# Kernel tuning notes

Measured on AMD Instinct MI355X. Metric: run time of the kernel, lower is better.

The kernel has to match this reference:

```python
import jax, jax.numpy as jnp
import numpy as np

B, S, F = 128, 32, 128
N_ACT = 19


def build_edge_index(S):
    """4-neighbor grid edges (directed both ways) + bidirectional meta-node edges."""
    idx = np.arange(S * S).reshape(S, S)
    src = np.concatenate([idx[:, :-1].ravel(), idx[:, 1:].ravel(), idx[:-1, :].ravel(), idx[1:, :].ravel()])
    dst = np.concatenate([idx[:, 1:].ravel(), idx[:, :-1].ravel(), idx[1:, :].ravel(), idx[:-1, :].ravel()])
    meta = S * S
    cells = np.arange(S * S)
    src = np.concatenate([src, cells, np.full(S * S, meta)])
    dst = np.concatenate([dst, np.full(S * S, meta), cells])
    return src.astype(np.int32), dst.astype(np.int32)


def setup_inputs() -> dict:
    key = jax.random.key(0)
    ks = jax.random.split(key, 16)
    g = lambda k, shape, fan: jax.random.normal(k, shape, jnp.float32) * (0.5 / np.sqrt(fan))
    return {
        "gmap": jax.random.normal(ks[0], (B, S, S, F), jnp.float32),
        "pos": jax.random.randint(ks[1], (B, 2), 0, S, jnp.int32),
        "action_mask": jax.random.randint(ks[2], (B, N_ACT), 0, 2, jnp.int32),
        "Ws": g(ks[3], (3, 128, 128), 128),
        "Wn": g(ks[4], (3, 128, 128), 128),
        "bs": jnp.zeros((3, 128), jnp.float32),
        "W_d1": g(ks[5], (640, 512), 640), "b_d1": jnp.zeros((512,), jnp.float32),
        "W_d2": g(ks[6], (512, 512), 512), "b_d2": jnp.zeros((512,), jnp.float32),
        "W_d3": g(ks[7], (512, 256), 512), "b_d3": jnp.zeros((256,), jnp.float32),
        "W_p1": g(ks[8], (256, 256), 256), "b_p1": jnp.zeros((256,), jnp.float32),
        "W_p2": g(ks[9], (256, 256), 256), "b_p2": jnp.zeros((256,), jnp.float32),
        "W_p3": g(ks[10], (256, 19), 256), "b_p3": jnp.zeros((19,), jnp.float32),
    }


def reference(gmap, pos, action_mask, Ws, Wn, bs,
              W_d1, b_d1, W_d2, b_d2, W_d3, b_d3,
              W_p1, b_p1, W_p2, b_p2, W_p3, b_p3):
    Bb, Ss = gmap.shape[0], gmap.shape[1]
    Ff = gmap.shape[3]
    src, dst = build_edge_index(Ss)  # constant edge structure (cache in original)
    # flatten map -> nodes, append zero meta node
    x = gmap.reshape(Bb, Ss * Ss, Ff)
    x = jnp.concatenate([x, jnp.zeros((Bb, 1, Ff), x.dtype)], axis=1)  # [B, N, F]
    # GNN tower: self + neighbor-sum message passing, ELU
    for l in range(Ws.shape[0]):
        agg = jnp.zeros_like(x).at[:, dst].add(x[:, src])  # scatter-add over edges
        x = jax.nn.elu(x @ Ws[l] + agg @ Wn[l] + bs[l])
    emb = x[:, :-1, :]  # drop meta node -> [B, S*S, D]
    D = emb.shape[-1]
    # pick_from_map: pad spatially by 1, gather 5 cells (N,W,S,E,center)
    m = emb.reshape(Bb, Ss, Ss, D)
    mpf = jnp.pad(m, ((0, 0), (1, 1), (1, 1), (0, 0))).reshape(Bb, (Ss + 2) * (Ss + 2), D)
    offsets = jnp.array([(-1, 0), (0, -1), (1, 0), (0, 1), (0, 0)], jnp.float32)
    o_pos = pos.astype(jnp.float32)[:, None, :] + offsets + 1.0  # [B, 5, 2]
    # NOTE: original uses stride map_size (S), not S+2, on the padded flat array
    j = (o_pos @ jnp.array([float(Ss), 1.0], jnp.float32)).astype(jnp.int32)  # [B, 5]
    picked = jnp.take_along_axis(mpf, j[:, :, None], axis=1)  # [B, 5, D]
    state = picked.reshape(Bb, 5 * D)
    # directions MLP
    h = jax.nn.elu(state @ W_d1 + b_d1)
    h = jax.nn.elu(h @ W_d2 + b_d2)
    feat = jax.nn.elu(h @ W_d3 + b_d3)
    # policy head + action mask
    p = jax.nn.elu(feat @ W_p1 + b_p1)
    p = jax.nn.elu(p @ W_p2 + b_p2)
    logits = p @ W_p3 + b_p3
    inf_mask = jnp.maximum(jnp.log(action_mask.astype(jnp.float32)),
                           jnp.finfo(jnp.float32).min)
    return logits + inf_mask
```

## Files before the change

### kernel.cpp

```cpp
#include <hip/hip_runtime.h>
#include <hip/hip_bf16.h>

#define BATCH 128
#define SGRID 32
#define NCELL 1024
#define NTOT  1025
#define FD    128
#define NACT  19
#define NEG_INF_F  (-3.4028234663852886e38f)
#define BF16_SAFE_F (3.3e38f)
#define XSTR 136

typedef unsigned short ushort_t;
typedef unsigned int   uint_t;
typedef short   short8   __attribute__((ext_vector_type(8)));
typedef float   floatx16 __attribute__((ext_vector_type(16)));

__device__ __forceinline__ float elu_fast(float v) {
    return v > 0.f ? v : (__expf(v) - 1.f);
}
__device__ __forceinline__ float bf2f(ushort_t h) {
    union { uint_t u; float f; } v; v.u = ((uint_t)h) << 16; return v.f;
}
__device__ __forceinline__ ushort_t f2bf(float f) {
    union { float f; uint_t u; } v; v.f = f;
    uint_t r = v.u + 0x7FFFu + ((v.u >> 16) & 1u);
    return (ushort_t)(r >> 16);
}
__device__ __forceinline__ uint_t pkbf(float a, float b) {
    union { __hip_bfloat162 h; uint_t u; } v;
    v.h = __float22bfloat162_rn(make_float2(a, b));
    return v.u;
}
__device__ __forceinline__ void unpack2(uint_t u, float& a, float& b) {
    union { uint_t x; float f; } lo, hi;
    lo.x = u << 16; hi.x = u & 0xFFFF0000u;
    a = lo.f; b = hi.f;
}
__device__ __forceinline__ void unpack8(uint4 v, float* f) {
    unpack2(v.x, f[0], f[1]); unpack2(v.y, f[2], f[3]);
    unpack2(v.z, f[4], f[5]); unpack2(v.w, f[6], f[7]);
}
__device__ __forceinline__ void unpack4(uint2 v, float* f) {
    unpack2(v.x, f[0], f[1]); unpack2(v.y, f[2], f[3]);
}

__global__ __launch_bounds__(256) void setup_kernel(
    const ushort_t* __restrict__ Ws,
    const ushort_t* __restrict__ Wn,
    ushort_t* __restrict__ wfrag,
    float* __restrict__ s0s1)
{
    const int g = blockIdx.x * 256 + threadIdx.x;
    if (g < 4096) {
        const int lane = g & 63;
        const int ks   = (g >> 6) & 7;
        const int nt   = (g >> 9) & 3;
        const int p    = (g >> 11) & 1;
        const ushort_t* W = p ? Wn : Ws;
        const int k0  = ks * 16 + (lane >> 5) * 8;
        const int col = nt * 32 + (lane & 31);
        ushort_t v[8];
        #pragma unroll
        for (int j = 0; j < 8; ++j) v[j] = W[(size_t)(k0 + j) * FD + col];
        uint4 u;
        u.x = v[0] | ((uint_t)v[1] << 16); u.y = v[2] | ((uint_t)v[3] << 16);
        u.z = v[4] | ((uint_t)v[5] << 16); u.w = v[6] | ((uint_t)v[7] << 16);
        *(uint4*)(wfrag + (size_t)g * 8) = u;
    } else {
        const int idx = g - 4096;
        float4 z = make_float4(0.f, 0.f, 0.f, 0.f);
        *(float4*)(s0s1 + (size_t)idx * 8)     = z;
        *(float4*)(s0s1 + (size_t)idx * 8 + 4) = z;
    }
}

__global__ __launch_bounds__(256, 4) void gnn_layer1(
    const ushort_t* __restrict__ xprev,
    ushort_t* __restrict__ xnext,
    const ushort_t* __restrict__ wfrag_layer,
    const ushort_t* __restrict__ bs,
    float* __restrict__ s0,
    float* __restrict__ s1)
{
    const int i = blockIdx.x;
    const int xcd = i & 7;
    const int j = i >> 3;
    const int b = xcd * 16 + (j >> 4);
    const int rb = j & 15;
    const int t = threadIdx.x;
    const ushort_t* xb = xprev + (size_t)b * (NCELL * FD);
    ushort_t* yb = xnext + (size_t)b * (NTOT * FD);

    __shared__ alignas(16) ushort_t xt[64 * XSTR];
    __shared__ alignas(16) ushort_t at[64 * XSTR];

    const int r0 = rb * 2;

    const ushort_t* src = xb + (size_t)(r0 * SGRID) * FD;
    uint4 mainT[4], haloT[4];
    const uint4 zero4 = make_uint4(0u, 0u, 0u, 0u);
    #pragma unroll
    for (int jj = 0; jj < 4; ++jj) {
        const int e8 = (t + 256 * jj) * 8;
        const int cc = e8 >> 7, k = e8 & 127;
        const int rr = cc >> 5, c = cc & 31;
        mainT[jj] = *(const uint4*)(src + e8);
        const int grow = (rr == 0) ? (r0 - 1) : (r0 + 2);
        haloT[jj] = (grow >= 0 && grow < SGRID)
            ? *(const uint4*)(xb + (size_t)(grow * SGRID + c) * FD + k) : zero4;
    }
    #pragma unroll
    for (int jj = 0; jj < 4; ++jj) {
        const int e8 = (t + 256 * jj) * 8;
        const int cc = e8 >> 7, k = e8 & 127;
        *(uint4*)&xt[cc * XSTR + k] = mainT[jj];
    }
    {
        float sp[8];
        #pragma unroll
        for (int q = 0; q < 8; ++q) sp[q] = 0.f;
        #pragma unroll
        for (int jj = 0; jj < 4; ++jj) {
            float f[8]; unpack8(mainT[jj], f);
            #pragma unroll
            for (int q = 0; q < 8; ++q) sp[q] += f[q];
        }
        float* atF = (float*)at;
        const int base = (t >> 4) * 128 + (t & 15) * 8;
        #pragma unroll
        for (int q = 0; q < 8; ++q) atF[base + q] = sp[q];
    }
    __syncthreads();
    if (t < 128) {
        const float* atF = (const float*)at;
        float s = 0.f;
        #pragma unroll
        for (int gI = 0; gI < 16; ++gI) s += atF[gI * 128 + t];
        atomicAdd(&s0[b * 128 + t], s);
    }
    __syncthreads();

    #pragma unroll
    for (int jj = 0; jj < 4; ++jj) {
        const int e8 = (t + 256 * jj) * 8;
        const int cc = e8 >> 7, k = e8 & 127;
        const int c = cc & 31;
        float s[8];
        unpack8(*(const uint4*)&xt[(cc ^ 32) * XSTR + k], s);
        if (c > 0) {
            float f[8]; unpack8(*(const uint4*)&xt[(cc - 1) * XSTR + k], f);
            #pragma unroll
            for (int q = 0; q < 8; ++q) s[q] += f[q];
        }
        if (c < 31) {
            float f[8]; unpack8(*(const uint4*)&xt[(cc + 1) * XSTR + k], f);
            #pragma unroll
            for (int q = 0; q < 8; ++q) s[q] += f[q];
        }
        {
            float f[8]; unpack8(haloT[jj], f);
            #pragma unroll
            for (int q = 0; q < 8; ++q) s[q] += f[q];
        }
        uint4 u;
        u.x = pkbf(s[0], s[1]); u.y = pkbf(s[2], s[3]);
        u.z = pkbf(s[4], s[5]); u.w = pkbf(s[6], s[7]);
        *(uint4*)&at[cc * XSTR + k] = u;
    }
    __syncthreads();

    const int w = t >> 6;
    const int l = t & 63;
    const int m0 = l & 31;
    const int koff = (l >> 5) * 8;

    floatx16 acc0, acc1;
    #pragma unroll
    for (int q = 0; q < 16; ++q) { acc0[q] = 0.f; acc1[q] = 0.f; }

    #pragma unroll
    for (int p = 0; p < 2; ++p) {
        const ushort_t* X = p ? at : xt;
        const ushort_t* WF = wfrag_layer + (size_t)((p * 4 + w) * 8) * 64 * 8;
        #pragma unroll
        for (int ks = 0; ks < 8; ++ks) {
            const short8 bfrag = *(const short8*)(WF + (size_t)(ks * 64 + l) * 8);
            const short8 a0 = *(const short8*)&X[m0 * XSTR + ks * 16 + koff];
            const short8 a1 = *(const short8*)&X[(m0 + 32) * XSTR + ks * 16 + koff];
            acc0 = __builtin_amdgcn_mfma_f32_32x32x16_bf16(a0, bfrag, acc0, 0, 0, 0);
            acc1 = __builtin_amdgcn_mfma_f32_32x32x16_bf16(a1, bfrag, acc1, 0, 0, 0);
        }
    }
    __syncthreads();

    const int col = w * 32 + (l & 31);
    const float bias = bf2f(bs[col]);
    float colsum = 0.f;
    #pragma unroll
    for (int mt = 0; mt < 2; ++mt) {
        const floatx16 A = mt ? acc1 : acc0;
        #pragma unroll
        for (int r = 0; r < 16; ++r) {
            const int rowC = (r & 3) + 8 * (r >> 2) + 4 * (l >> 5);
            const float v = elu_fast(A[r] + bias);
            colsum += v;
            xt[(mt * 32 + rowC) * XSTR + col] = f2bf(v);
        }
    }
    ((float*)at)[col * 2 + (l >> 5)] = colsum;
    __syncthreads();
    if (t < 128) {
        const float* atF = (const float*)at;
        atomicAdd(&s1[b * 128 + t], atF[t * 2] + atF[t * 2 + 1]);
    }
    ushort_t* dst = yb + (size_t)(r0 * SGRID) * FD;
    #pragma unroll
    for (int jj = 0; jj < 4; ++jj) {
        const int e8 = (t + 256 * jj) * 8;
        const int cc = e8 >> 7, k = e8 & 127;
        *(uint4*)(dst + e8) = *(const uint4*)&xt[cc * XSTR + k];
    }
}

__global__ __launch_bounds__(256) void head_window(
    const ushort_t* __restrict__ x1g,
    const int* __restrict__ pos,
    const ushort_t* __restrict__ Ws,
    const ushort_t* __restrict__ Wn,
    const ushort_t* __restrict__ bs,
    const float* __restrict__ s0,
    const float* __restrict__ s1,
    float* __restrict__ stg)
{
    const int xcd = blockIdx.x & 7;
    const int idx = blockIdx.x >> 3;
    const int b = xcd * 16 + idx / 5;
    const int g = idx % 5;
    const int t = threadIdx.x;
    const int f = t & 127;
    const int h = t >> 7;

    const int D13R[13] = {-2,-1,-1,-1, 0, 0, 0, 0, 0, 1, 1, 1, 2};
    const int D13C[13] = { 0,-1, 0, 1,-2,-1, 0, 1, 2,-1, 0, 1, 0};
    const int C5[5]    = { 2, 5, 6, 7, 9 };

    __shared__ float x1d[13 * 128];
    __shared__ float x2d[5 * 128];
    __shared__ float aggd[5 * 128];
    __shared__ float m1[128], m2[128], agg3[128];
    __shared__ float part[2][128];

    const int OFFR[5] = {-1, 0, 1, 0, 0};
    const int OFFC[5] = {0, -1, 0, 1, 0};
    const int pr = pos[b * 2 + 0] + OFFR[g];
    const int pc = pos[b * 2 + 1] + OFFC[g];

    const ushort_t* Ws2 = Ws + FD * FD;
    const ushort_t* Wn2 = Wn + FD * FD;
    const ushort_t* Ws3 = Ws + 2 * FD * FD;
    const ushort_t* Wn3 = Wn + 2 * FD * FD;

    for (int e = t; e < 13 * 128; e += 256) {
        const int ci = e >> 7, ff = e & 127;
        const int r = pr + D13R[ci], c = pc + D13C[ci];
        float v = 0.f;
        if (r >= 0 && r < SGRID && c >= 0 && c < SGRID)
            v = bf2f(x1g[((size_t)b * NTOT + r * SGRID + c) * FD + ff]);
        x1d[ci * 128 + ff] = v;
    }
    {
        float a = 0.f;
        const int kb = h * 64;
        #pragma unroll 8
        for (int k = kb; k < kb + 64; ++k)
            a += s0[b * 128 + k] * bf2f(Wn[k * FD + f]);
        part[h][f] = a;
    }
    __syncthreads();
    if (t < 128) m1[f] = elu_fast(bf2f(bs[f]) + part[0][f] + part[1][f]);
    __syncthreads();
    {
        float a = 0.f;
        const int kb = h * 64;
        #pragma unroll 4
        for (int k = kb; k < kb + 64; ++k)
            a += m1[k] * bf2f(Ws2[k * FD + f]) + s1[b * 128 + k] * bf2f(Wn2[k * FD + f]);
        part[h][f] = a;
    }
    __syncthreads();
    if (t < 128) m2[f] = elu_fast(bf2f(bs[FD + f]) + part[0][f] + part[1][f]);
    for (int e = t; e < 5 * 128; e += 256) {
        const int cc = e >> 7, ff = e & 127;
        const int dr = D13R[C5[cc]], dc = D13C[C5[cc]];
        float a = 0.f;
        #pragma unroll
        for (int d = 0; d < 4; ++d) {
            const int DR[4] = {-1, 1, 0, 0};
            const int DC[4] = {0, 0, -1, 1};
            const int nr = dr + DR[d], nc = dc + DC[d];
            #pragma unroll
            for (int ci = 0; ci < 13; ++ci)
                if (D13R[ci] == nr && D13C[ci] == nc) a += x1d[ci * 128 + ff];
        }
        aggd[e] = a;
    }
    __syncthreads();
    for (int e = t; e < 5 * 128; e += 256) aggd[e] += m1[e & 127];
    __syncthreads();
    for (int cc = h; cc < 5; cc += 2) {
        const int ci = C5[cc];
        float a = bf2f(bs[FD + f]);
        #pragma unroll 4
        for (int k = 0; k < 128; ++k)
            a += x1d[ci * 128 + k] * bf2f(Ws2[k * FD + f])
               + aggd[cc * 128 + k] * bf2f(Wn2[k * FD + f]);
        x2d[cc * 128 + f] = elu_fast(a);
    }
    __syncthreads();
    if (t < 128) {
        float a = m2[f];
        const int DR[4] = {-1, 1, 0, 0};
        const int DC[4] = {0, 0, -1, 1};
        const int CCn[4] = {0, 4, 1, 3};
        #pragma unroll
        for (int d = 0; d < 4; ++d) {
            const int r = pr + DR[d], c = pc + DC[d];
            if (r >= 0 && r < SGRID && c >= 0 && c < SGRID)
                a += x2d[CCn[d] * 128 + f];
        }
        agg3[f] = a;
    }
    __syncthreads();
    {
        float a = 0.f;
        const int kb = h * 64;
        #pragma unroll 4
        for (int k = kb; k < kb + 64; ++k)
            a += x2d[2 * 128 + k] * bf2f(Ws3[k * FD + f])
               + agg3[k] * bf2f(Wn3[k * FD + f]);
        part[h][f] = a;
    }
    __syncthreads();
    if (t < 128) {
        const bool ig = (pr >= 0 && pr < SGRID && pc >= 0 && pc < SGRID);
        const float v = elu_fast(bf2f(bs[2 * FD + f]) + part[0][f] + part[1][f]);
        stg[(size_t)b * 640 + g * 128 + f] = ig ? v : 0.f;
    }
}

__global__ __launch_bounds__(1024) void head_mlp(
    const float* __restrict__ stg,
    const int* __restrict__ amask,
    const ushort_t* __restrict__ Wd1, const ushort_t* __restrict__ bd1,
    const ushort_t* __restrict__ Wd2, const ushort_t* __restrict__ bd2,
    const ushort_t* __restrict__ Wd3, const ushort_t* __restrict__ bd3,
    const ushort_t* __restrict__ Wp1, const ushort_t* __restrict__ bp1,
    const ushort_t* __restrict__ Wp2, const ushort_t* __restrict__ bp2,
    const ushort_t* __restrict__ Wp3, const ushort_t* __restrict__ bp3,
    ushort_t* __restrict__ out)
{
    const int t = threadIdx.x;
    const int b = (blockIdx.x & 7) * 16 + (blockIdx.x >> 3);
    const int q = t >> 6;
    const int lane = t & 63;

    __shared__ float st[640];
    __shared__ float bufA[512];
    __shared__ float bufB[512];
    __shared__ float part[16][512];

    if (t < 640) st[t] = stg[(size_t)b * 640 + t];
    __syncthreads();

    {
        float acc[8];
        #pragma unroll
        for (int p = 0; p < 8; ++p) acc[p] = 0.f;
        const int c0 = lane * 8;
        const int kb = q * 40;
        #pragma unroll 8
        for (int k = kb; k < kb + 40; ++k) {
            const float s = st[k];
            float fv[8]; unpack8(*(const uint4*)(Wd1 + (size_t)k * 512 + c0), fv);
            #pragma unroll
            for (int p = 0; p < 8; ++p) acc[p] += s * fv[p];
        }
        #pragma unroll
        for (int p = 0; p < 8; ++p) part[q][c0 + p] = acc[p];
        __syncthreads();
        if (t < 512) {
            float a = bf2f(bd1[t]);
            #pragma unroll
            for (int p = 0; p < 16; ++p) a += part[p][t];
            bufA[t] = elu_fast(a);
        }
        __syncthreads();
    }
    {
        float acc[8];
        #pragma unroll
        for (int p = 0; p < 8; ++p) acc[p] = 0.f;
        const int c0 = lane * 8;
        const int kb = q * 32;
        #pragma unroll 8
        for (int k = kb; k < kb + 32; ++k) {
            const float s = bufA[k];
            float fv[8]; unpack8(*(const uint4*)(Wd2 + (size_t)k * 512 + c0), fv);
            #pragma unroll
            for (int p = 0; p < 8; ++p) acc[p] += s * fv[p];
        }
        #pragma unroll
        for (int p = 0; p < 8; ++p) part[q][c0 + p] = acc[p];
        __syncthreads();
        if (t < 512) {
            float a = bf2f(bd2[t]);
            #pragma unroll
            for (int p = 0; p < 16; ++p) a += part[p][t];
            bufB[t] = elu_fast(a);
        }
        __syncthreads();
    }
    {
        float acc[4];
        #pragma unroll
        for (int p = 0; p < 4; ++p) acc[p] = 0.f;
        const int c0 = lane * 4;
        const int kb = q * 32;
        #pragma unroll 8
        for (int k = kb; k < kb + 32; ++k) {
            const float s = bufB[k];
            float fv[4]; unpack4(*(const uint2*)(Wd3 + (size_t)k * 256 + c0), fv);
            #pragma unroll
            for (int p = 0; p < 4; ++p) acc[p] += s * fv[p];
        }
        #pragma unroll
        for (int p = 0; p < 4; ++p) part[q][c0 + p] = acc[p];
        __syncthreads();
        if (t < 256) {
            float a = bf2f(bd3[t]);
            #pragma unroll
            for (int p = 0; p < 16; ++p) a += part[p][t];
            st[t] = elu_fast(a);
        }
        __syncthreads();
    }
    {
        float acc[4];
        #pragma unroll
        for (int p = 0; p < 4; ++p) acc[p] = 0.f;
        const int c0 = lane * 4;
        const int kb = q * 16;
        #pragma unroll 8
        for (int k = kb; k < kb + 16; ++k) {
            const float s = st[k];
            float fv[4]; unpack4(*(const uint2*)(Wp1 + (size_t)k * 256 + c0), fv);
            #pragma unroll
            for (int p = 0; p < 4; ++p) acc[p] += s * fv[p];
        }
        #pragma unroll
        for (int p = 0; p < 4; ++p) part[q][c0 + p] = acc[p];
        __syncthreads();
        if (t < 256) {
            float a = bf2f(bp1[t]);
            #pragma unroll
            for (int p = 0; p < 16; ++p) a += part[p][t];
            bufA[t] = elu_fast(a);
        }
        __syncthreads();
    }
    {
        float acc[4];
        #pragma unroll
        for (int p = 0; p < 4; ++p) acc[p] = 0.f;
        const int c0 = lane * 4;
        const int kb = q * 16;
        #pragma unroll 8
        for (int k = kb; k < kb + 16; ++k) {
            const float s = bufA[k];
            float fv[4]; unpack4(*(const uint2*)(Wp2 + (size_t)k * 256 + c0), fv);
            #pragma unroll
            for (int p = 0; p < 4; ++p) acc[p] += s * fv[p];
        }
        #pragma unroll
        for (int p = 0; p < 4; ++p) part[q][c0 + p] = acc[p];
        __syncthreads();
        if (t < 256) {
            float a = bf2f(bp2[t]);
            #pragma unroll
            for (int p = 0; p < 16; ++p) a += part[p][t];
            bufB[t] = elu_fast(a);
        }
        __syncthreads();
    }
    {
        float a = 0.f;
        const int kb = q * 16;
        if (lane < NACT) {
            #pragma unroll 8
            for (int k = kb; k < kb + 16; ++k)
                a += bufB[k] * bf2f(Wp3[(size_t)k * NACT + lane]);
            part[q][lane] = a;
        }
        __syncthreads();
        if (t < NACT) {
            float v = bf2f(bp3[t]);
            #pragma unroll
            for (int p = 0; p < 16; ++p) v += part[p][t];
            v += amask[b * NACT + t] ? 0.f : NEG_INF_F;
            v = fminf(fmaxf(v, -BF16_SAFE_F), BF16_SAFE_F);
            out[b * NACT + t] = f2bf(v);
        }
    }
}

extern "C" void kernel_launch(void* const* d_in, const int* in_sizes, int n_in,
                              void* d_out, int out_size, void* d_ws, size_t ws_size,
                              hipStream_t stream) {
    const ushort_t* gmap  = (const ushort_t*)d_in[0];
    const int*      pos   = (const int*)     d_in[1];
    const int*      amask = (const int*)     d_in[2];
    const ushort_t* Ws    = (const ushort_t*)d_in[3];
    const ushort_t* Wn    = (const ushort_t*)d_in[4];
    const ushort_t* bs    = (const ushort_t*)d_in[5];
    const ushort_t* Wd1   = (const ushort_t*)d_in[6];
    const ushort_t* bd1   = (const ushort_t*)d_in[7];
    const ushort_t* Wd2   = (const ushort_t*)d_in[8];
    const ushort_t* bd2   = (const ushort_t*)d_in[9];
    const ushort_t* Wd3   = (const ushort_t*)d_in[10];
    const ushort_t* bd3   = (const ushort_t*)d_in[11];
    const ushort_t* Wp1   = (const ushort_t*)d_in[12];
    const ushort_t* bp1   = (const ushort_t*)d_in[13];
    const ushort_t* Wp2   = (const ushort_t*)d_in[14];
    const ushort_t* bp2   = (const ushort_t*)d_in[15];
    const ushort_t* Wp3   = (const ushort_t*)d_in[16];
    const ushort_t* bp3   = (const ushort_t*)d_in[17];

    ushort_t* x1 = (ushort_t*)d_ws;
    ushort_t* wfrag = x1 + (size_t)BATCH * NTOT * FD;
    float* s0s1 = (float*)(wfrag + 4096 * 8);
    float* s0 = s0s1;
    float* s1 = s0s1 + BATCH * FD;
    float* stg = s0s1 + 2 * BATCH * FD;

    setup_kernel<<<32, 256, 0, stream>>>(Ws, Wn, wfrag, s0s1);

    gnn_layer1<<<16 * BATCH, 256, 0, stream>>>(gmap, x1, wfrag, bs, s0, s1);

    head_window<<<640, 256, 0, stream>>>(x1, pos, Ws, Wn, bs, s0, s1, stg);

    head_mlp<<<BATCH, 1024, 0, stream>>>(stg, amask,
                                         Wd1, bd1, Wd2, bd2, Wd3, bd3,
                                         Wp1, bp1, Wp2, bp2, Wp3, bp3,
                                         (ushort_t*)d_out);
}
```

Before: 206.9 us.

## Restructure head_window as split-K GEMV with 512 threads and vector weight loads

The head_window kernel moves from 256 to 512 threads. Each thread now handles 4 output columns over an 8-row K slice, using packed bf16 vector loads (uint2/uint4), and 16 partial sums are reduced through shared memory. The neighbor aggregation becomes explicit index sums, and the five center-cell layer-2 matvecs share weight loads instead of re-reading weights per cell. The aim is to cut serial per-thread weight-load latency in this small kernel, at the cost of more shared memory, more barriers (one per output cell in the reduction loop), and reliance on unpack helpers that are assumed to exist.

```diff
diff --git a/kernel.cpp b/kernel.cpp
--- a/kernel.cpp
+++ b/kernel.cpp
@@ -223,7 +223,7 @@
     }
 }
 
-__global__ __launch_bounds__(256) void head_window(
+__global__ __launch_bounds__(512) void head_window(
     const ushort_t* __restrict__ x1g,
     const int* __restrict__ pos,
     const ushort_t* __restrict__ Ws,
@@ -239,113 +239,177 @@
     const int g = idx % 5;
     const int t = threadIdx.x;
     const int f = t & 127;
-    const int h = t >> 7;
-
-    const int D13R[13] = {-2,-1,-1,-1, 0, 0, 0, 0, 0, 1, 1, 1, 2};
-    const int D13C[13] = { 0,-1, 0, 1,-2,-1, 0, 1, 2,-1, 0, 1, 0};
-    const int C5[5]    = { 2, 5, 6, 7, 9 };
-
-    __shared__ float x1d[13 * 128];
-    __shared__ float x2d[5 * 128];
-    __shared__ float aggd[5 * 128];
+    const int cg = t & 31;
+    const int c0 = cg * 4;
+    const int kg = t >> 5;
+    const int k0 = kg * 8;
+
+    __shared__ float x1d[13][128];
+    __shared__ float x2d[5][128];
+    __shared__ float aggd[5][128];
     __shared__ float m1[128], m2[128], agg3[128];
-    __shared__ float part[2][128];
+    __shared__ float s0L[128], s1L[128];
+    __shared__ float part[16][128];
 
     const int OFFR[5] = {-1, 0, 1, 0, 0};
     const int OFFC[5] = {0, -1, 0, 1, 0};
     const int pr = pos[b * 2 + 0] + OFFR[g];
     const int pc = pos[b * 2 + 1] + OFFC[g];
 
+    const ushort_t* Wn1 = Wn;
     const ushort_t* Ws2 = Ws + FD * FD;
     const ushort_t* Wn2 = Wn + FD * FD;
     const ushort_t* Ws3 = Ws + 2 * FD * FD;
     const ushort_t* Wn3 = Wn + 2 * FD * FD;
 
-    for (int e = t; e < 13 * 128; e += 256) {
-        const int ci = e >> 7, ff = e & 127;
-        const int r = pr + D13R[ci], c = pc + D13C[ci];
-        float v = 0.f;
-        if (r >= 0 && r < SGRID && c >= 0 && c < SGRID)
-            v = bf2f(x1g[((size_t)b * NTOT + r * SGRID + c) * FD + ff]);
-        x1d[ci * 128 + ff] = v;
-    }
-    {
-        float a = 0.f;
-        const int kb = h * 64;
-        #pragma unroll 8
-        for (int k = kb; k < kb + 64; ++k)
-            a += s0[b * 128 + k] * bf2f(Wn[k * FD + f]);
-        part[h][f] = a;
-    }
-    __syncthreads();
-    if (t < 128) m1[f] = elu_fast(bf2f(bs[f]) + part[0][f] + part[1][f]);
-    __syncthreads();
-    {
-        float a = 0.f;
-        const int kb = h * 64;
-        #pragma unroll 4
-        for (int k = kb; k < kb + 64; ++k)
-            a += m1[k] * bf2f(Ws2[k * FD + f]) + s1[b * 128 + k] * bf2f(Wn2[k * FD + f]);
-        part[h][f] = a;
-    }
-    __syncthreads();
-    if (t < 128) m2[f] = elu_fast(bf2f(bs[FD + f]) + part[0][f] + part[1][f]);
-    for (int e = t; e < 5 * 128; e += 256) {
-        const int cc = e >> 7, ff = e & 127;
-        const int dr = D13R[C5[cc]], dc = D13C[C5[cc]];
-        float a = 0.f;
-        #pragma unroll
-        for (int d = 0; d < 4; ++d) {
-            const int DR[4] = {-1, 1, 0, 0};
-            const int DC[4] = {0, 0, -1, 1};
-            const int nr = dr + DR[d], nc = dc + DC[d];
-            #pragma unroll
-            for (int ci = 0; ci < 13; ++ci)
-                if (D13R[ci] == nr && D13C[ci] == nc) a += x1d[ci * 128 + ff];
-        }
-        aggd[e] = a;
-    }
-    __syncthreads();
-    for (int e = t; e < 5 * 128; e += 256) aggd[e] += m1[e & 127];
-    __syncthreads();
-    for (int cc = h; cc < 5; cc += 2) {
-        const int ci = C5[cc];
+    if (t < 128)      s0L[t] = s0[b * 128 + t];
+    else if (t < 256) s1L[t - 128] = s1[b * 128 + (t - 128)];
+    {
+        const int D13R[13] = {-2,-1,-1,-1, 0, 0, 0, 0, 0, 1, 1, 1, 2};
+        const int D13C[13] = { 0,-1, 0, 1,-2,-1, 0, 1, 2,-1, 0, 1, 0};
+        if (t < 208) {
+            const int ci = t >> 4, kq = (t & 15) * 8;
+            const int r = pr + D13R[ci], c = pc + D13C[ci];
+            float fv[8];
+            if (r >= 0 && r < SGRID && c >= 0 && c < SGRID) {
+                unpack8(*(const uint4*)(x1g + ((size_t)b * NTOT + r * SGRID + c) * FD + kq), fv);
+            } else {
+                #pragma unroll
+                for (int jq = 0; jq < 8; ++jq) fv[jq] = 0.f;
+            }
+            #pragma unroll
+            for (int jq = 0; jq < 8; ++jq) x1d[ci][kq + jq] = fv[jq];
+        }
+    }
+    __syncthreads();
+
+    {
+        float acc[4] = {0.f, 0.f, 0.f, 0.f};
+        #pragma unroll
+        for (int i = 0; i < 8; ++i) {
+            const int k = k0 + i;
+            float wv[4]; unpack4(*(const uint2*)(Wn1 + k * FD + c0), wv);
+            const float sv = s0L[k];
+            #pragma unroll
+            for (int jq = 0; jq < 4; ++jq) acc[jq] += sv * wv[jq];
+        }
+        #pragma unroll
+        for (int jq = 0; jq < 4; ++jq) part[kg][c0 + jq] = acc[jq];
+    }
+    __syncthreads();
+    if (t < 128) {
+        float a = bf2f(bs[f]);
+        #pragma unroll
+        for (int p = 0; p < 16; ++p) a += part[p][f];
+        m1[f] = elu_fast(a);
+    }
+    __syncthreads();
+
+    {
+        float acc[4] = {0.f, 0.f, 0.f, 0.f};
+        #pragma unroll
+        for (int i = 0; i < 8; ++i) {
+            const int k = k0 + i;
+            float wsv[4], wnv[4];
+            unpack4(*(const uint2*)(Ws2 + k * FD + c0), wsv);
+            unpack4(*(const uint2*)(Wn2 + k * FD + c0), wnv);
+            const float mv = m1[k], sv = s1L[k];
+            #pragma unroll
+            for (int jq = 0; jq < 4; ++jq) acc[jq] += mv * wsv[jq] + sv * wnv[jq];
+        }
+        #pragma unroll
+        for (int jq = 0; jq < 4; ++jq) part[kg][c0 + jq] = acc[jq];
+    }
+    __syncthreads();
+    if (t < 128) {
         float a = bf2f(bs[FD + f]);
-        #pragma unroll 4
-        for (int k = 0; k < 128; ++k)
-            a += x1d[ci * 128 + k] * bf2f(Ws2[k * FD + f])
-               + aggd[cc * 128 + k] * bf2f(Wn2[k * FD + f]);
-        x2d[cc * 128 + f] = elu_fast(a);
-    }
-    __syncthreads();
+        #pragma unroll
+        for (int p = 0; p < 16; ++p) a += part[p][f];
+        m2[f] = elu_fast(a);
+    }
     if (t < 128) {
-        float a = m2[f];
-        const int DR[4] = {-1, 1, 0, 0};
-        const int DC[4] = {0, 0, -1, 1};
-        const int CCn[4] = {0, 4, 1, 3};
-        #pragma unroll
-        for (int d = 0; d < 4; ++d) {
-            const int r = pr + DR[d], c = pc + DC[d];
-            if (r >= 0 && r < SGRID && c >= 0 && c < SGRID)
-                a += x2d[CCn[d] * 128 + f];
-        }
-        agg3[f] = a;
-    }
-    __syncthreads();
-    {
-        float a = 0.f;
-        const int kb = h * 64;
-        #pragma unroll 4
-        for (int k = kb; k < kb + 64; ++k)
-            a += x2d[2 * 128 + k] * bf2f(Ws3[k * FD + f])
-               + agg3[k] * bf2f(Wn3[k * FD + f]);
-        part[h][f] = a;
+        const float mm = m1[t];
+        aggd[0][t] = x1d[0][t]  + x1d[6][t]  + x1d[1][t] + x1d[3][t]  + mm;
+        aggd[1][t] = x1d[1][t]  + x1d[9][t]  + x1d[4][t] + x1d[6][t]  + mm;
+        aggd[2][t] = x1d[2][t]  + x1d[10][t] + x1d[5][t] + x1d[7][t]  + mm;
+        aggd[3][t] = x1d[3][t]  + x1d[11][t] + x1d[6][t] + x1d[8][t]  + mm;
+        aggd[4][t] = x1d[6][t]  + x1d[12][t] + x1d[9][t] + x1d[11][t] + mm;
+    }
+    __syncthreads();
+
+    {
+        float acc[5][4];
+        #pragma unroll
+        for (int cc = 0; cc < 5; ++cc)
+            #pragma unroll
+            for (int jq = 0; jq < 4; ++jq) acc[cc][jq] = 0.f;
+        #pragma unroll
+        for (int i = 0; i < 8; ++i) {
+            const int k = k0 + i;
+            float wsv[4], wnv[4];
+            unpack4(*(const uint2*)(Ws2 + k * FD + c0), wsv);
+            unpack4(*(const uint2*)(Wn2 + k * FD + c0), wnv);
+            const float xv0 = x1d[2][k],  av0 = aggd[0][k];
+            const float xv1 = x1d[5][k],  av1 = aggd[1][k];
+            const float xv2 = x1d[6][k],  av2 = aggd[2][k];
+            const float xv3 = x1d[7][k],  av3 = aggd[3][k];
+            const float xv4 = x1d[10][k], av4 = aggd[4][k];
+            #pragma unroll
+            for (int jq = 0; jq < 4; ++jq) {
+                acc[0][jq] += xv0 * wsv[jq] + av0 * wnv[jq];
+                acc[1][jq] += xv1 * wsv[jq] + av1 * wnv[jq];
+                acc[2][jq] += xv2 * wsv[jq] + av2 * wnv[jq];
+                acc[3][jq] += xv3 * wsv[jq] + av3 * wnv[jq];
+                acc[4][jq] += xv4 * wsv[jq] + av4 * wnv[jq];
+            }
+        }
+        #pragma unroll
+        for (int cc = 0; cc < 5; ++cc) {
+            #pragma unroll
+            for (int jq = 0; jq < 4; ++jq) part[kg][c0 + jq] = acc[cc][jq];
+            __syncthreads();
+            if (t < 128) {
+                float a = bf2f(bs[FD + f]);
+                #pragma unroll
+                for (int p = 0; p < 16; ++p) a += part[p][f];
+                x2d[cc][f] = elu_fast(a);
+            }
+            __syncthreads();
+        }
+    }
+
+    if (t < 128) {
+        float a = m2[t];
+        if (pr - 1 >= 0)    a += x2d[0][t];
+        if (pr + 1 < SGRID) a += x2d[4][t];
+        if (pc - 1 >= 0)    a += x2d[1][t];
+        if (pc + 1 < SGRID) a += x2d[3][t];
+        agg3[t] = a;
+    }
+    __syncthreads();
+
+    {
+        float acc[4] = {0.f, 0.f, 0.f, 0.f};
+        #pragma unroll
+        for (int i = 0; i < 8; ++i) {
+            const int k = k0 + i;
+            float wsv[4], wnv[4];
+            unpack4(*(const uint2*)(Ws3 + k * FD + c0), wsv);
+            unpack4(*(const uint2*)(Wn3 + k * FD + c0), wnv);
+            const float xv = x2d[2][k], av = agg3[k];
+            #pragma unroll
+            for (int jq = 0; jq < 4; ++jq) acc[jq] += xv * wsv[jq] + av * wnv[jq];
+        }
+        #pragma unroll
+        for (int jq = 0; jq < 4; ++jq) part[kg][c0 + jq] = acc[jq];
     }
     __syncthreads();
     if (t < 128) {
         const bool ig = (pr >= 0 && pr < SGRID && pc >= 0 && pc < SGRID);
-        const float v = elu_fast(bf2f(bs[2 * FD + f]) + part[0][f] + part[1][f]);
-        stg[(size_t)b * 640 + g * 128 + f] = ig ? v : 0.f;
+        float a = bf2f(bs[2 * FD + f]);
+        #pragma unroll
+        for (int p = 0; p < 16; ++p) a += part[p][f];
+        stg[(size_t)b * 640 + g * 128 + f] = ig ? elu_fast(a) : 0.f;
     }
 }
 
@@ -547,7 +611,7 @@
 
     gnn_layer1<<<16 * BATCH, 256, 0, stream>>>(gmap, x1, wfrag, bs, s0, s1);
 
-    head_window<<<640, 256, 0, stream>>>(x1, pos, Ws, Wn, bs, s0, s1, stg);
+    head_window<<<640, 512, 0, stream>>>(x1, pos, Ws, Wn, bs, s0, s1, stg);
 
     head_mlp<<<BATCH, 1024, 0, stream>>>(stg, amask,
                                          Wd1, bd1, Wd2, bd2, Wd3, bd3,
```

After: 188.6 us. 1.1x faster.
